# Kernel tuning notes

Hardware: AMD Instinct MI355X
Metric: run time of the kernel (lower is better)

## Reference

```python
import jax, jax.numpy as jnp
import numpy as np

EPS = 1e-8  # F.cosine_similarity eps
K = 2       # prompt_length


def setup_inputs() -> dict:
    key = jax.random.key(0)
    k1, k2, k3, k4 = jax.random.split(key, 4)
    B, DIM, NP, D = 32, 64, 4, 1024   # P: [batch, dim, N_p, D]; D == V (rows of stored table)
    E, VC = 768, 32000                 # stored table [V=D, E]; f_e: E -> vocab_dim=VC
    P = jax.random.normal(k1, (B, DIM, NP, D), dtype=jnp.float32)
    we_stored = jax.random.normal(k2, (D, E), dtype=jnp.float32) * 0.02
    fe_w = jax.random.normal(k3, (VC, E), dtype=jnp.float32) * 0.02
    fe_b = jax.random.normal(k4, (VC,), dtype=jnp.float32) * 0.02
    return {"P": P, "we_stored": we_stored, "fe_w": fe_w, "fe_b": fe_b}


def reference(P, we_stored, fe_w, fe_b):
    # word_embeddings = f_e(stored).t()  ->  [vocab_dim, V] == [VC, D]
    T = (we_stored @ fe_w.T + fe_b).T            # [VC, D]
    B, DIM, NP, D = P.shape
    # Cosine sim of each tiled embedding row (repeated N_p times) vs flattened P_i:
    #   dot(tiled_w, P_flat) = w . sum_j P[..., j, :]
    #   ||tiled_w|| = sqrt(N_p) * ||w||
    s = P.sum(axis=2)                                             # [B, DIM, D]
    w_norm = jnp.maximum(jnp.sqrt(jnp.float32(NP)) * jnp.linalg.norm(T, axis=1), EPS)   # [VC]
    p_norm = jnp.maximum(jnp.linalg.norm(P.reshape(B, DIM, -1), axis=-1), EPS)          # [B, DIM]
    scores = jnp.einsum('bdk,vk->bdv', s, T) / (w_norm[None, None, :] * p_norm[..., None])  # [B, DIM, VC]
    values, indices = jax.lax.top_k(scores, K)                    # [B, DIM, K]
    e_k = T[indices]                                              # [B, DIM, K, D]
    Z = jnp.concatenate([e_k, P], axis=2)                         # [B, DIM, NP+K, D]
    return Z, values
```

## Files before the change

### kernel.cpp

```cpp
#include <hip/hip_runtime.h>
#include <hip/hip_bf16.h>
#include <math.h>

#define B_    32
#define DIM_  64
#define NP_   4
#define D_    1024
#define E_    768
#define VC_   32000
#define R_    2048
#define KTOP  2
#define EPS_  1e-8f
#define NCB   250
#define NCAND 8

#define T_OFF    ((size_t)0)
#define S_OFF    (T_OFF + (size_t)VC_ * D_)
#define INVW_OFF (S_OFF + (size_t)R_ * D_)
#define INVP_OFF (INVW_OFF + VC_)
#define WSQ_OFF  (INVP_OFF + R_)
#define PV_OFF   (WSQ_OFF + VC_)
#define PI_OFF   (PV_OFF + (size_t)R_ * NCB * 2)
#define SB_OFF   (PI_OFF + (size_t)R_ * NCB * 2)
#define TB_OFF   (SB_OFF + (size_t)R_ * D_ / 2)
#define WH_OFF   (TB_OFF + (size_t)VC_ * D_ / 2)
#define WL_OFF   (WH_OFF + (size_t)D_ * E_ / 2)
#define CAND_OFF (WL_OFF + (size_t)D_ * E_ / 2)
#define TIDX_OFF (CAND_OFF + (size_t)R_ * NCAND)

#define NEG_INF (-3.4e38f)

typedef __bf16 bf16x8 __attribute__((ext_vector_type(8)));
typedef unsigned short u16x8 __attribute__((ext_vector_type(8)));
typedef float  f32x4  __attribute__((ext_vector_type(4)));

__device__ __forceinline__ unsigned short f2bf(float f) {
    unsigned u = __float_as_uint(f);
    u += 0x7fffu + ((u >> 16) & 1u);
    return (unsigned short)(u >> 16);
}

__device__ __forceinline__ void async_ld16(const void* gptr, void* lptr) {
    __builtin_amdgcn_global_load_lds(
        (const __attribute__((address_space(1))) void*)(uintptr_t)gptr,
        (__attribute__((address_space(3))) void*)(unsigned)(uintptr_t)lptr,
        16, 0, 0);
}

__device__ __forceinline__ bool better(float v, int i, float bv, int bi) {
    return (v > bv) || (v == bv && i < bi);
}

__global__ __launch_bounds__(256) void k_zero(float* __restrict__ wsq) {
    int i = blockIdx.x * 256 + threadIdx.x;
    if (i < VC_) wsq[i] = 0.f;
}

__global__ __launch_bounds__(256) void k_split_we(const float* __restrict__ x,
                                                  unsigned short* __restrict__ hi,
                                                  unsigned short* __restrict__ lo) {
    int i = (blockIdx.x * 256 + threadIdx.x) * 4;
    float4 v = *(const float4*)(x + i);
    ushort4 h, l;
    float e;
    h.x = f2bf(v.x); e = v.x - __uint_as_float((unsigned)h.x << 16); l.x = f2bf(e);
    h.y = f2bf(v.y); e = v.y - __uint_as_float((unsigned)h.y << 16); l.y = f2bf(e);
    h.z = f2bf(v.z); e = v.z - __uint_as_float((unsigned)h.z << 16); l.z = f2bf(e);
    h.w = f2bf(v.w); e = v.w - __uint_as_float((unsigned)h.w << 16); l.w = f2bf(e);
    *(ushort4*)(hi + i) = h;
    *(ushort4*)(lo + i) = l;
}

__global__ __launch_bounds__(256) void k_sum_pnorm(const float* __restrict__ P,
                                                   float* __restrict__ s,
                                                   unsigned short* __restrict__ sb,
                                                   float* __restrict__ invp) {
    int r = blockIdx.x;
    int t = threadIdx.x;
    const float* base = P + (size_t)r * NP_ * D_;
    float4 acc = make_float4(0.f, 0.f, 0.f, 0.f);
    float sq = 0.f;
#pragma unroll
    for (int np = 0; np < NP_; ++np) {
        float4 v = *(const float4*)(base + (size_t)np * D_ + t * 4);
        acc.x += v.x; acc.y += v.y; acc.z += v.z; acc.w += v.w;
        sq += v.x * v.x + v.y * v.y + v.z * v.z + v.w * v.w;
    }
    *(float4*)(s + (size_t)r * D_ + t * 4) = acc;
    ushort4 o;
    o.x = f2bf(acc.x); o.y = f2bf(acc.y); o.z = f2bf(acc.z); o.w = f2bf(acc.w);
    *(ushort4*)(sb + (size_t)r * D_ + t * 4) = o;

    __shared__ float red[256];
    red[t] = sq;
    __syncthreads();
    for (int off = 128; off > 0; off >>= 1) {
        if (t < off) red[t] += red[t + off];
        __syncthreads();
    }
    if (t == 0) invp[r] = 1.0f / fmaxf(sqrtf(red[0]), EPS_);
}

__global__ __launch_bounds__(256) void k_gemm_T_mfma(const float* __restrict__ A,
                                                     const unsigned short* __restrict__ Bh,
                                                     const unsigned short* __restrict__ Bl,
                                                     const float* __restrict__ bias,
                                                     float* __restrict__ T,
                                                     unsigned short* __restrict__ Tb,
                                                     float* __restrict__ wsq) {
    __shared__ __align__(16) float          Af[128 * 32];
    __shared__ __align__(16) unsigned short Bsh[128 * 32];
    __shared__ __align__(16) unsigned short Bsl[128 * 32];

    int tid = threadIdx.x;
    int wid = tid >> 6, lane = tid & 63;
    int quad = lane >> 4, l15 = lane & 15;
    int v0 = blockIdx.y * 128;
    int d0 = blockIdx.x * 128;
    int vband = (wid & 1) * 64, nband = (wid >> 1) * 64;

    f32x4 acc[4][4];
#pragma unroll
    for (int i = 0; i < 4; ++i)
#pragma unroll
        for (int j = 0; j < 4; ++j) acc[i][j] = f32x4{0.f, 0.f, 0.f, 0.f};

    int arow = wid * 32 + (lane >> 3);
    int acol = (lane & 7) * 4;
    int brow = wid * 32 + (lane >> 2);
    int bcol = (lane & 3) * 8;

    for (int k0 = 0; k0 < E_; k0 += 32) {
#pragma unroll
        for (int j = 0; j < 4; ++j)
            async_ld16(A + (size_t)(v0 + arow + j * 8) * E_ + k0 + acol,
                       (void*)(Af + (wid * 32 + j * 8) * 32));
#pragma unroll
        for (int j = 0; j < 2; ++j) {
            async_ld16(Bh + (size_t)(d0 + brow + j * 16) * E_ + k0 + bcol,
                       (void*)(Bsh + (wid * 32 + j * 16) * 32));
            async_ld16(Bl + (size_t)(d0 + brow + j * 16) * E_ + k0 + bcol,
                       (void*)(Bsl + (wid * 32 + j * 16) * 32));
        }
        __syncthreads();

        bf16x8 bh[4], bl[4];
#pragma unroll
        for (int nt = 0; nt < 4; ++nt) {
            bh[nt] = *(const bf16x8*)(Bsh + (nband + nt * 16 + l15) * 32 + quad * 8);
            bl[nt] = *(const bf16x8*)(Bsl + (nband + nt * 16 + l15) * 32 + quad * 8);
        }
#pragma unroll
        for (int mt = 0; mt < 4; ++mt) {
            const float* ap = Af + (vband + mt * 16 + l15) * 32 + quad * 8;
            f32x4 xa = *(const f32x4*)ap;
            f32x4 xb = *(const f32x4*)(ap + 4);
            bf16x8 ah, al;
#pragma unroll
            for (int e = 0; e < 4; ++e) {
                __bf16 h0 = (__bf16)xa[e];
                __bf16 h1 = (__bf16)xb[e];
                ah[e] = h0; ah[e + 4] = h1;
                al[e]     = (__bf16)(xa[e] - (float)h0);
                al[e + 4] = (__bf16)(xb[e] - (float)h1);
            }
#pragma unroll
            for (int nt = 0; nt < 4; ++nt) {
                acc[mt][nt] = __builtin_amdgcn_mfma_f32_16x16x32_bf16(ah, bh[nt], acc[mt][nt], 0, 0, 0);
                acc[mt][nt] = __builtin_amdgcn_mfma_f32_16x16x32_bf16(al, bh[nt], acc[mt][nt], 0, 0, 0);
                acc[mt][nt] = __builtin_amdgcn_mfma_f32_16x16x32_bf16(ah, bl[nt], acc[mt][nt], 0, 0, 0);
            }
        }
        __syncthreads();
    }

    float sq[4][4] = {};
#pragma unroll
    for (int mt = 0; mt < 4; ++mt) {
        int vbase = v0 + vband + mt * 16 + quad * 4;
        float bv[4];
#pragma unroll
        for (int rg = 0; rg < 4; ++rg) bv[rg] = bias[vbase + rg];
#pragma unroll
        for (int nt = 0; nt < 4; ++nt) {
            int d = d0 + nband + nt * 16 + l15;
#pragma unroll
            for (int rg = 0; rg < 4; ++rg) {
                float val = acc[mt][nt][rg] + bv[rg];
                T[(size_t)(vbase + rg) * D_ + d] = val;
                __bf16 vb = (__bf16)val;
                Tb[(size_t)(vbase + rg) * D_ + d] = __builtin_bit_cast(unsigned short, vb);
                sq[mt][rg] += val * val;
            }
        }
    }
#pragma unroll
    for (int mt = 0; mt < 4; ++mt)
#pragma unroll
        for (int rg = 0; rg < 4; ++rg) {
            float p = sq[mt][rg];
            p += __shfl_xor(p, 1); p += __shfl_xor(p, 2);
            p += __shfl_xor(p, 4); p += __shfl_xor(p, 8);
            if (l15 == 0) atomicAdd(&wsq[v0 + vband + mt * 16 + quad * 4 + rg], p);
        }
}

__global__ __launch_bounds__(256) void k_invw(const float* __restrict__ wsq,
                                              float* __restrict__ invw) {
    int v = blockIdx.x * 256 + threadIdx.x;
    if (v < VC_) invw[v] = 1.0f / fmaxf(2.0f * sqrtf(wsq[v]), EPS_);
}

__global__ __launch_bounds__(256) void k_scores_mfma(const unsigned short* __restrict__ Tb,
                                                     const unsigned short* __restrict__ sb,
                                                     const float* __restrict__ invw,
                                                     float* __restrict__ pval,
                                                     int* __restrict__ pidx) {
    __shared__ __align__(16) unsigned short As[128 * 32];
    __shared__ __align__(16) unsigned short Bs[128 * 32];
    __shared__ float mv[2][128][2];
    __shared__ int   mi[2][128][2];

    int tid = threadIdx.x;
    int wid = tid >> 6, lane = tid & 63;
    int quad = lane >> 4, l15 = lane & 15;
    int v0 = blockIdx.x * 128;
    int r0 = blockIdx.y * 128;
    int vband = (wid & 1) * 64, rband = (wid >> 1) * 64;

    f32x4 acc[4][4];
#pragma unroll
    for (int i = 0; i < 4; ++i)
#pragma unroll
        for (int j = 0; j < 4; ++j) acc[i][j] = f32x4{0.f, 0.f, 0.f, 0.f};

    int srow  = wid * 32 + (lane >> 2);
    int skoff = (lane & 3) * 8;

    for (int k0 = 0; k0 < D_; k0 += 32) {
#pragma unroll
        for (int j = 0; j < 2; ++j) {
            async_ld16(Tb + (size_t)(v0 + srow + j * 16) * D_ + k0 + skoff,
                       (void*)(As + (wid * 32 + j * 16) * 32));
            async_ld16(sb + (size_t)(r0 + srow + j * 16) * D_ + k0 + skoff,
                       (void*)(Bs + (wid * 32 + j * 16) * 32));
        }
        __syncthreads();
        bf16x8 af[4], bf[4];
#pragma unroll
        for (int mt = 0; mt < 4; ++mt)
            af[mt] = *(const bf16x8*)(As + (vband + mt * 16 + l15) * 32 + quad * 8);
#pragma unroll
        for (int nt = 0; nt < 4; ++nt)
            bf[nt] = *(const bf16x8*)(Bs + (rband + nt * 16 + l15) * 32 + quad * 8);
#pragma unroll
        for (int mt = 0; mt < 4; ++mt)
#pragma unroll
            for (int nt = 0; nt < 4; ++nt)
                acc[mt][nt] = __builtin_amdgcn_mfma_f32_16x16x32_bf16(af[mt], bf[nt], acc[mt][nt], 0, 0, 0);
        __syncthreads();
    }

    float iw[4][4];
#pragma unroll
    for (int mt = 0; mt < 4; ++mt)
#pragma unroll
        for (int rg = 0; rg < 4; ++rg)
            iw[mt][rg] = invw[v0 + vband + mt * 16 + quad * 4 + rg];

#pragma unroll
    for (int nt = 0; nt < 4; ++nt) {
        float b1 = NEG_INF, b2 = NEG_INF;
        int i1 = 0x7fffffff, i2 = 0x7fffffff;
#pragma unroll
        for (int mt = 0; mt < 4; ++mt)
#pragma unroll
            for (int rg = 0; rg < 4; ++rg) {
                float val = acc[mt][nt][rg] * iw[mt][rg];
                int v = v0 + vband + mt * 16 + quad * 4 + rg;
                if (better(val, v, b1, i1)) { b2 = b1; i2 = i1; b1 = val; i1 = v; }
                else if (better(val, v, b2, i2)) { b2 = val; i2 = v; }
            }
#pragma unroll
        for (int off = 16; off <= 32; off <<= 1) {
            float o1 = __shfl_xor(b1, off), o2 = __shfl_xor(b2, off);
            int  oi1 = __shfl_xor(i1, off), oi2 = __shfl_xor(i2, off);
            if (better(o1, oi1, b1, i1)) {
                if (better(b1, i1, o2, oi2)) { b2 = b1; i2 = i1; } else { b2 = o2; i2 = oi2; }
                b1 = o1; i1 = oi1;
            } else if (better(o1, oi1, b2, i2)) { b2 = o1; i2 = oi1; }
        }
        if (quad == 0) {
            int rl = rband + nt * 16 + l15;
            mv[wid & 1][rl][0] = b1; mi[wid & 1][rl][0] = i1;
            mv[wid & 1][rl][1] = b2; mi[wid & 1][rl][1] = i2;
        }
    }
    __syncthreads();
    if (tid < 128) {
        float b1 = mv[0][tid][0], b2 = mv[0][tid][1];
        int   i1 = mi[0][tid][0], i2 = mi[0][tid][1];
#pragma unroll
        for (int sl = 0; sl < 2; ++sl) {
            float o = mv[1][tid][sl]; int oi = mi[1][tid][sl];
            if (better(o, oi, b1, i1)) { b2 = b1; i2 = i1; b1 = o; i1 = oi; }
            else if (better(o, oi, b2, i2)) { b2 = o; i2 = oi; }
        }
        size_t off = ((size_t)(r0 + tid) * NCB + blockIdx.x) * 2;
        pval[off] = b1;     pidx[off] = i1;
        pval[off + 1] = b2; pidx[off + 1] = i2;
    }
}

__global__ __launch_bounds__(256) void k_topk8(const float* __restrict__ pval,
                                               const int* __restrict__ pidx,
                                               int* __restrict__ cands) {
    int r = blockIdx.x, t = threadIdx.x;
    __shared__ float v[512];
    __shared__ int  id[512];
    for (int c = t; c < 512; c += 256) {
        if (c < NCB * 2) { v[c] = pval[(size_t)r * NCB * 2 + c]; id[c] = pidx[(size_t)r * NCB * 2 + c]; }
        else             { v[c] = NEG_INF; id[c] = 0x7fffffff; }
    }
    __syncthreads();
    if (t == 0) {
        float bv[NCAND]; int bi[NCAND];
#pragma unroll
        for (int j = 0; j < NCAND; ++j) { bv[j] = NEG_INF; bi[j] = 0x7fffffff; }
        for (int c = 0; c < NCB * 2; ++c) {
            float x = v[c]; int xi = id[c];
            if (better(x, xi, bv[NCAND - 1], bi[NCAND - 1])) {
                int j = NCAND - 1;
                while (j > 0 && better(x, xi, bv[j - 1], bi[j - 1])) {
                    bv[j] = bv[j - 1]; bi[j] = bi[j - 1]; --j;
                }
                bv[j] = x; bi[j] = xi;
            }
        }
#pragma unroll
        for (int j = 0; j < NCAND; ++j) cands[r * NCAND + j] = bi[j];
    }
}

__global__ __launch_bounds__(256) void k_rescore(const float* __restrict__ s,
                                                 const float* __restrict__ T,
                                                 const int* __restrict__ cands,
                                                 const float* __restrict__ invw,
                                                 const float* __restrict__ invp,
                                                 float* __restrict__ outv,
                                                 int* __restrict__ tidx) {
    int r = blockIdx.x, t = threadIdx.x;
    int cg = t >> 5, l32 = t & 31;
    int c = cands[r * NCAND + cg];
    const float* Trow = T + (size_t)c * D_;
    const float* srow = s + (size_t)r * D_;
    float p = 0.f;
#pragma unroll
    for (int j = 0; j < 8; ++j) {
        int e = (j * 32 + l32) * 4;
        float4 a = *(const float4*)(srow + e);
        float4 b = *(const float4*)(Trow + e);
        p += a.x * b.x + a.y * b.y + a.z * b.z + a.w * b.w;
    }
#pragma unroll
    for (int off = 16; off >= 1; off >>= 1) p += __shfl_xor(p, off);
    __shared__ float sc[NCAND];
    if (l32 == 0) sc[cg] = p;
    __syncthreads();
    if (t == 0) {
        float ip = invp[r];
        float b1 = NEG_INF, b2 = NEG_INF;
        int i1 = 0x7fffffff, i2 = 0x7fffffff;
#pragma unroll
        for (int j = 0; j < NCAND; ++j) {
            int ci = cands[r * NCAND + j];
            float val = sc[j] * invw[ci] * ip;
            if (better(val, ci, b1, i1)) { b2 = b1; i2 = i1; b1 = val; i1 = ci; }
            else if (better(val, ci, b2, i2)) { b2 = val; i2 = ci; }
        }
        outv[(size_t)r * 2 + 0] = b1;
        outv[(size_t)r * 2 + 1] = b2;
        tidx[r * 2 + 0] = i1;
        tidx[r * 2 + 1] = i2;
    }
}

__global__ __launch_bounds__(256) void k_writeZ(const float* __restrict__ P,
                                                const float* __restrict__ T,
                                                const int* __restrict__ tidx,
                                                float* __restrict__ out) {
    int blk = blockIdx.x;
    int r = blk / 6, j = blk - r * 6;
    const float* src;
    if (j < KTOP) src = T + (size_t)tidx[r * 2 + j] * D_;
    else          src = P + ((size_t)r * NP_ + (j - KTOP)) * D_;
    float4 v = *(const float4*)(src + threadIdx.x * 4);
    *(float4*)(out + ((size_t)r * 6 + j) * D_ + threadIdx.x * 4) = v;
}

extern "C" void kernel_launch(void* const* d_in, const int* in_sizes, int n_in,
                              void* d_out, int out_size, void* d_ws, size_t ws_size,
                              hipStream_t stream) {
    const float* P   = (const float*)d_in[0];
    const float* we  = (const float*)d_in[1];
    const float* few = (const float*)d_in[2];
    const float* feb = (const float*)d_in[3];
    float* out = (float*)d_out;
    float* ws  = (float*)d_ws;

    float* T    = ws + T_OFF;
    float* s    = ws + S_OFF;
    float* invw = ws + INVW_OFF;
    float* invp = ws + INVP_OFF;
    float* wsq  = ws + WSQ_OFF;
    float* pval = ws + PV_OFF;
    int*   pidx = (int*)(ws + PI_OFF);
    unsigned short* sb  = (unsigned short*)(ws + SB_OFF);
    unsigned short* Tb  = (unsigned short*)(ws + TB_OFF);
    unsigned short* weh = (unsigned short*)(ws + WH_OFF);
    unsigned short* wel = (unsigned short*)(ws + WL_OFF);
    int*   cands = (int*)(ws + CAND_OFF);
    int*   tidx  = (int*)(ws + TIDX_OFF);
    float* outv = out + (size_t)R_ * 6 * D_;

    k_zero<<<(VC_ + 255) / 256, 256, 0, stream>>>(wsq);
    k_split_we<<<(D_ * E_) / 1024, 256, 0, stream>>>(we, weh, wel);
    k_sum_pnorm<<<R_, 256, 0, stream>>>(P, s, sb, invp);
    k_gemm_T_mfma<<<dim3(D_ / 128, VC_ / 128), 256, 0, stream>>>(few, weh, wel, feb, T, Tb, wsq);
    k_invw<<<(VC_ + 255) / 256, 256, 0, stream>>>(wsq, invw);
    k_scores_mfma<<<dim3(VC_ / 128, R_ / 128), 256, 0, stream>>>(Tb, sb, invw, pval, pidx);
    k_topk8<<<R_, 256, 0, stream>>>(pval, pidx, cands);
    k_rescore<<<R_, 256, 0, stream>>>(s, T, cands, invw, invp, outv, tidx);
    k_writeZ<<<R_ * 6, 256, 0, stream>>>(P, T, tidx, out);
}
```

Before: 710.5 us.

## Double-buffer scores GEMM LDS, swizzle LDS slots, and remap blocks for XCD locality

The scores GEMM now double-buffers its shared-memory tiles, prefetching the next K-slice while MFMAs run on the current one. The LDS column slot is rotated per row pair to reduce bank conflicts. Both GEMMs switch to a 1D grid whose block index is remapped by id&7 into contiguous tile ranges, intended to keep neighbouring tiles on the same XCD and improve L2 reuse. This adds LDS use, which may lower occupancy, and the prefetch relies on the single barrier per iteration being correct.

Result: faster. 683.1 us (-3.9%).

```diff
diff --git a/kernel.cpp b/kernel.cpp
--- a/kernel.cpp
+++ b/kernel.cpp
@@ -115,8 +115,10 @@
     int tid = threadIdx.x;
     int wid = tid >> 6, lane = tid & 63;
     int quad = lane >> 4, l15 = lane & 15;
-    int v0 = blockIdx.y * 128;
-    int d0 = blockIdx.x * 128;
+    int id  = blockIdx.x;
+    int swz = (id & 7) * 250 + (id >> 3);
+    int v0 = (swz >> 3) * 128;
+    int d0 = (swz & 7) * 128;
     int vband = (wid & 1) * 64, nband = (wid >> 1) * 64;
 
     f32x4 acc[4][4];
@@ -216,16 +218,20 @@
                                                      const float* __restrict__ invw,
                                                      float* __restrict__ pval,
                                                      int* __restrict__ pidx) {
-    __shared__ __align__(16) unsigned short As[128 * 32];
-    __shared__ __align__(16) unsigned short Bs[128 * 32];
+    __shared__ __align__(16) unsigned short As[2][128 * 32];
+    __shared__ __align__(16) unsigned short Bs[2][128 * 32];
     __shared__ float mv[2][128][2];
     __shared__ int   mi[2][128][2];
 
     int tid = threadIdx.x;
     int wid = tid >> 6, lane = tid & 63;
     int quad = lane >> 4, l15 = lane & 15;
-    int v0 = blockIdx.x * 128;
-    int r0 = blockIdx.y * 128;
+    int id   = blockIdx.x;
+    int swz  = (id & 7) * 500 + (id >> 3);
+    int vblk = swz >> 4;
+    int rblk = swz & 15;
+    int v0 = vblk * 128;
+    int r0 = rblk * 128;
     int vband = (wid & 1) * 64, rband = (wid >> 1) * 64;
 
     f32x4 acc[4][4];
@@ -234,31 +240,50 @@
 #pragma unroll
         for (int j = 0; j < 4; ++j) acc[i][j] = f32x4{0.f, 0.f, 0.f, 0.f};
 
-    int srow  = wid * 32 + (lane >> 2);
-    int skoff = (lane & 3) * 8;
+    int r_lane = lane >> 2;
+    int slot   = lane & 3;
+
+#define STAGE_SC(buf, kk)                                                          \
+    {                                                                              \
+_Pragma("unroll")                                                                  \
+        for (int j = 0; j < 2; ++j) {                                              \
+            int rowt = wid * 32 + j * 16 + r_lane;                                 \
+            int ss = (slot - (rowt >> 1)) & 3;                                     \
+            async_ld16(Tb + (size_t)(v0 + rowt) * D_ + (kk) + ss * 8,              \
+                       (void*)(As[buf] + (wid * 32 + j * 16) * 32));               \
+            async_ld16(sb + (size_t)(r0 + rowt) * D_ + (kk) + ss * 8,              \
+                       (void*)(Bs[buf] + (wid * 32 + j * 16) * 32));               \
+        }                                                                          \
+    }
+
+    int cur = 0;
+    STAGE_SC(0, 0);
+    __syncthreads();
 
     for (int k0 = 0; k0 < D_; k0 += 32) {
-#pragma unroll
-        for (int j = 0; j < 2; ++j) {
-            async_ld16(Tb + (size_t)(v0 + srow + j * 16) * D_ + k0 + skoff,
-                       (void*)(As + (wid * 32 + j * 16) * 32));
-            async_ld16(sb + (size_t)(r0 + srow + j * 16) * D_ + k0 + skoff,
-                       (void*)(Bs + (wid * 32 + j * 16) * 32));
-        }
+        if (k0 + 32 < D_) STAGE_SC(cur ^ 1, k0 + 32);
+
+        bf16x8 af[4], bfr[4];
+#pragma unroll
+        for (int mt = 0; mt < 4; ++mt) {
+            int row = vband + mt * 16 + l15;
+            int ps = (quad + (row >> 1)) & 3;
+            af[mt] = *(const bf16x8*)(As[cur] + row * 32 + ps * 8);
+        }
+#pragma unroll
+        for (int nt = 0; nt < 4; ++nt) {
+            int row = rband + nt * 16 + l15;
+            int ps = (quad + (row >> 1)) & 3;
+            bfr[nt] = *(const bf16x8*)(Bs[cur] + row * 32 + ps * 8);
+        }
+#pragma unroll
+        for (int mt = 0; mt < 4; ++mt)
+#pragma unroll
+            for (int nt = 0; nt < 4; ++nt)
+                acc[mt][nt] = __builtin_amdgcn_mfma_f32_16x16x32_bf16(af[mt], bfr[nt], acc[mt][nt], 0, 0, 0);
+
         __syncthreads();
-        bf16x8 af[4], bf[4];
-#pragma unroll
-        for (int mt = 0; mt < 4; ++mt)
-            af[mt] = *(const bf16x8*)(As + (vband + mt * 16 + l15) * 32 + quad * 8);
-#pragma unroll
-        for (int nt = 0; nt < 4; ++nt)
-            bf[nt] = *(const bf16x8*)(Bs + (rband + nt * 16 + l15) * 32 + quad * 8);
-#pragma unroll
-        for (int mt = 0; mt < 4; ++mt)
-#pragma unroll
-            for (int nt = 0; nt < 4; ++nt)
-                acc[mt][nt] = __builtin_amdgcn_mfma_f32_16x16x32_bf16(af[mt], bf[nt], acc[mt][nt], 0, 0, 0);
-        __syncthreads();
+        cur ^= 1;
     }
 
     float iw[4][4];
@@ -306,10 +331,11 @@
             if (better(o, oi, b1, i1)) { b2 = b1; i2 = i1; b1 = o; i1 = oi; }
             else if (better(o, oi, b2, i2)) { b2 = o; i2 = oi; }
         }
-        size_t off = ((size_t)(r0 + tid) * NCB + blockIdx.x) * 2;
+        size_t off = ((size_t)(r0 + tid) * NCB + vblk) * 2;
         pval[off] = b1;     pidx[off] = i1;
         pval[off + 1] = b2; pidx[off + 1] = i2;
     }
+#undef STAGE_SC
 }
 
 __global__ __launch_bounds__(256) void k_topk8(const float* __restrict__ pval,
@@ -426,9 +452,9 @@
     k_zero<<<(VC_ + 255) / 256, 256, 0, stream>>>(wsq);
     k_split_we<<<(D_ * E_) / 1024, 256, 0, stream>>>(we, weh, wel);
     k_sum_pnorm<<<R_, 256, 0, stream>>>(P, s, sb, invp);
-    k_gemm_T_mfma<<<dim3(D_ / 128, VC_ / 128), 256, 0, stream>>>(few, weh, wel, feb, T, Tb, wsq);
+    k_gemm_T_mfma<<<2000, 256, 0, stream>>>(few, weh, wel, feb, T, Tb, wsq);
     k_invw<<<(VC_ + 255) / 256, 256, 0, stream>>>(wsq, invw);
-    k_scores_mfma<<<dim3(VC_ / 128, R_ / 128), 256, 0, stream>>>(Tb, sb, invw, pval, pidx);
+    k_scores_mfma<<<4000, 256, 0, stream>>>(Tb, sb, invw, pval, pidx);
     k_topk8<<<R_, 256, 0, stream>>>(pval, pidx, cands);
     k_rescore<<<R_, 256, 0, stream>>>(s, T, cands, invw, invp, outv, tidx);
     k_writeZ<<<R_ * 6, 256, 0, stream>>>(P, T, tidx, out);
```
